# Kernel tuning notes

Measured on AMD Instinct MI355X. Metric: run time of the kernel, lower is better.

The kernel has to match this reference:

```python
import jax, jax.numpy as jnp
import numpy as np

GAMMA = 1.0

def setup_inputs() -> dict:
    key = jax.random.key(0)
    kq, kk, kv = jax.random.split(key, 3)
    B, N, M, D = 4, 2048, 2048, 128
    q = jax.random.normal(kq, (B, N, D), dtype=jnp.float32)
    k = jax.random.normal(kk, (B, M, D), dtype=jnp.float32)
    v = jax.random.normal(kv, (B, M, D), dtype=jnp.float32)
    return {"q": q, "k": k, "v": v}

def reference(q, k, v):
    # RBF attention: weights = softmax(-gamma * ||q_i - k_j||^2, axis=-1)
    # dist2 via expansion ||q||^2 + ||k||^2 - 2 q.k (same math as broadcast-subtract,
    # avoids materializing the [B,N,M,D] tensor the torch code builds).
    q2 = jnp.sum(q * q, axis=-1)                    # [B,N]
    k2 = jnp.sum(k * k, axis=-1)                    # [B,M]
    qk = jnp.einsum('bnd,bmd->bnm', q, k)           # [B,N,M]
    dist2 = q2[:, :, None] + k2[:, None, :] - 2.0 * qk
    weights = jax.nn.softmax(-GAMMA * dist2, axis=-1)  # [B,N,M]
    return jnp.einsum('bnm,bmd->bnd', weights, v)      # [B,N,D]
```

## Files before the change

kernel.cpp:

```cpp
#include <hip/hip_runtime.h>
#include <hip/hip_bf16.h>

#define B_ 4
#define N_ 2048
#define M_ 2048
#define D_ 128
#define QBLK 128
#define NTHREADS 256
#define KVBLK 64
#define NTILES 32
#define TILE_BYTES 16384
#define SPLIT_MAX 8

typedef __attribute__((ext_vector_type(8))) short short8;
typedef __attribute__((ext_vector_type(16))) float floatx16;
typedef __attribute__((ext_vector_type(4))) unsigned int u32x4;
typedef unsigned short u16;
typedef unsigned int u32;

__device__ __forceinline__ u16 f2bf(float x) {
  u32 u = __builtin_bit_cast(u32, x);
  u32 r = (u + 0x7FFFu + ((u >> 16) & 1u)) >> 16;
  return (u16)r;
}
__device__ __forceinline__ float bf2f(u16 h) {
  u32 u = ((u32)h) << 16;
  return __builtin_bit_cast(float, u);
}
__device__ __forceinline__ u32 cvtpk(float a, float b) {
  u32 r;
  asm("v_cvt_pk_bf16_f32 %0, %1, %2" : "=v"(r) : "v"(a), "v"(b));
  return r;
}

#define GLOAD16(src, dst)                                                     \
  __builtin_amdgcn_global_load_lds(                                           \
      (const __attribute__((address_space(1))) void*)(src),                   \
      (__attribute__((address_space(3))) void*)(dst), 16, 0, 0)

__global__ __launch_bounds__(256) void prep_kernel(
    const float* __restrict__ k, const float* __restrict__ v,
    u16* __restrict__ khi_g, u16* __restrict__ klo_g,
    u16* __restrict__ vt_g, float* __restrict__ k2_g)
{
  __shared__ u16 T[64][136];
  int tid = threadIdx.x;
  if (blockIdx.x < 512) {
    int gid = blockIdx.x * 256 + tid;
    int row_g = gid >> 4;
    int j = gid & 15;
    const float* kp = k + (size_t)row_g * D_ + j * 8;
    float4 a = *(const float4*)kp;
    float4 c = *(const float4*)(kp + 4);
    float xs[8] = {a.x, a.y, a.z, a.w, c.x, c.y, c.z, c.w};
    short8 hi, lo;
    float ss = 0.f;
    #pragma unroll
    for (int e = 0; e < 8; ++e) {
      ss += xs[e] * xs[e];
      float x2 = 2.f * xs[e];
      u16 h = f2bf(x2);
      hi[e] = (short)h;
      lo[e] = (short)f2bf(x2 - bf2f(h));
    }
    ss += __shfl_xor(ss, 1);
    ss += __shfl_xor(ss, 2);
    ss += __shfl_xor(ss, 4);
    ss += __shfl_xor(ss, 8);
    if (j == 0) k2_g[row_g] = ss;
    int m = row_g & (M_ - 1);
    int b = row_g >> 11;
    int tile = m >> 6, r = m & 63;
    size_t base = ((size_t)b * NTILES + tile) * TILE_BYTES;
    u32 off = (u32)(r * 256 + j * 16) ^ ((u32)(r & 7) << 4);
    *(short8*)((char*)khi_g + base + off) = hi;
    *(short8*)((char*)klo_g + base + off) = lo;
  } else {
    int blk = blockIdx.x - 512;
    int b = blk >> 5, tile = blk & 31;
    const float* vp = v + ((size_t)b * M_ + tile * 64) * D_;
    #pragma unroll
    for (int p = 0; p < 8; ++p) {
      int idx = p * 256 + tid;
      int r = idx >> 5, c4 = idx & 31;
      float4 vv = *(const float4*)(vp + (size_t)r * D_ + c4 * 4);
      T[r][c4 * 4 + 0] = f2bf(vv.x);
      T[r][c4 * 4 + 1] = f2bf(vv.y);
      T[r][c4 * 4 + 2] = f2bf(vv.z);
      T[r][c4 * 4 + 3] = f2bf(vv.w);
    }
    __syncthreads();
    size_t base = ((size_t)b * NTILES + tile) * TILE_BYTES;
    #pragma unroll
    for (int p = 0; p < 4; ++p) {
      int idx = p * 256 + tid;
      int d = idx >> 3, rb = idx & 7;
      short8 s;
      #pragma unroll
      for (int i = 0; i < 8; ++i) s[i] = (short)T[rb * 8 + i][d];
      u32 off = (u32)(d * 128 + rb * 16) ^ ((u32)(d & 7) << 4);
      *(short8*)((char*)vt_g + base + off) = s;
    }
  }
}

__global__ __launch_bounds__(NTHREADS, 2) void rbf_attn_kernel(
    const float* __restrict__ q, const u16* __restrict__ khi_g,
    const u16* __restrict__ klo_g, const u16* __restrict__ vt_g,
    const float* __restrict__ k2_g, float* __restrict__ out,
    float* __restrict__ Opart, float* __restrict__ mpart,
    float* __restrict__ lpart, int nsplit, int tiles_per_split)
{
  __shared__ __align__(16) u16 KhiL[64 * 128];
  __shared__ __align__(16) u16 KloL[64 * 128];
  __shared__ __align__(16) u16 VtL[128 * 64];
  __shared__ __align__(16) float k2L[64];

  const int tid = threadIdx.x;
  const int w = tid >> 6;
  const int lane = tid & 63;
  const int qlc = lane & 31;
  const int h = lane >> 5;
  const int b = blockIdx.y;
  const int qt = blockIdx.x;
  const int sp = blockIdx.z;
  const int q0 = qt * QBLK;
  const int kt0 = sp * tiles_per_split, kt1 = kt0 + tiles_per_split;

  short8 Qh[8], Ql[8];
  {
    const float* qp = q + ((size_t)b * N_ + q0 + w * 32 + qlc) * D_ + h * 8;
    #pragma unroll
    for (int s = 0; s < 8; ++s) {
      float4 a = *(const float4*)(qp + s * 16);
      float4 c = *(const float4*)(qp + s * 16 + 4);
      float xs[8] = {a.x, a.y, a.z, a.w, c.x, c.y, c.z, c.w};
      #pragma unroll
      for (int j = 0; j < 8; ++j) {
        u16 hi = f2bf(xs[j]);
        Qh[s][j] = (short)hi;
        Ql[s][j] = (short)f2bf(xs[j] - bf2f(hi));
      }
    }
  }

  const char* khi_b = (const char*)khi_g + (size_t)b * NTILES * TILE_BYTES;
  const char* klo_b = (const char*)klo_g + (size_t)b * NTILES * TILE_BYTES;
  const char* vt_b = (const char*)vt_g + (size_t)b * NTILES * TILE_BYTES;
  const float* k2_b = k2_g + (size_t)b * M_;

  floatx16 o[4];
  #pragma unroll
  for (int dt = 0; dt < 4; ++dt) o[dt] = (floatx16)0.0f;
  float mrun = -1e30f, lrun = 0.f;

  for (int kt = kt0; kt < kt1; ++kt) {
    __syncthreads();
    {
      const char* kh = khi_b + (size_t)kt * TILE_BYTES;
      const char* kl = klo_b + (size_t)kt * TILE_BYTES;
      const char* vt = vt_b + (size_t)kt * TILE_BYTES;
      const int so = tid * 16;
      #pragma unroll
      for (int c = 0; c < 4; ++c) {
        GLOAD16(kh + c * 4096 + so, (char*)KhiL + c * 4096 + w * 1024);
        GLOAD16(kl + c * 4096 + so, (char*)KloL + c * 4096 + w * 1024);
        GLOAD16(vt + c * 4096 + so, (char*)VtL + c * 4096 + w * 1024);
      }
      if (tid < 16)
        GLOAD16((const char*)(k2_b + kt * KVBLK) + tid * 16, (char*)k2L);
    }
    asm volatile("s_waitcnt vmcnt(0)" ::: "memory");
    __syncthreads();

    floatx16 accS0 = (floatx16)0.0f, accS1 = (floatx16)0.0f;
    __builtin_amdgcn_s_setprio(1);
    #pragma unroll
    for (int s = 0; s < 8; ++s) {
      {
        int row = qlc;
        u32 off = ((u32)(row * 256 + s * 32 + h * 16)) ^ ((u32)(row & 7) << 4);
        short8 ah = *(const short8*)((const char*)KhiL + off);
        short8 al = *(const short8*)((const char*)KloL + off);
        accS0 = __builtin_amdgcn_mfma_f32_32x32x16_bf16(ah, Qh[s], accS0, 0, 0, 0);
        accS0 = __builtin_amdgcn_mfma_f32_32x32x16_bf16(al, Qh[s], accS0, 0, 0, 0);
        accS0 = __builtin_amdgcn_mfma_f32_32x32x16_bf16(ah, Ql[s], accS0, 0, 0, 0);
      }
      {
        int row = 32 + qlc;
        u32 off = ((u32)(row * 256 + s * 32 + h * 16)) ^ ((u32)(row & 7) << 4);
        short8 ah = *(const short8*)((const char*)KhiL + off);
        short8 al = *(const short8*)((const char*)KloL + off);
        accS1 = __builtin_amdgcn_mfma_f32_32x32x16_bf16(ah, Qh[s], accS1, 0, 0, 0);
        accS1 = __builtin_amdgcn_mfma_f32_32x32x16_bf16(al, Qh[s], accS1, 0, 0, 0);
        accS1 = __builtin_amdgcn_mfma_f32_32x32x16_bf16(ah, Ql[s], accS1, 0, 0, 0);
      }
    }
    __builtin_amdgcn_s_setprio(0);

    float mx = -3e38f;
    #pragma unroll
    for (int ct = 0; ct < 2; ++ct) {
      #pragma unroll
      for (int g = 0; g < 4; ++g) {
        float4 kq = *(const float4*)&k2L[32 * ct + 8 * g + 4 * h];
        if (ct == 0) {
          accS0[4 * g + 0] -= kq.x; accS0[4 * g + 1] -= kq.y;
          accS0[4 * g + 2] -= kq.z; accS0[4 * g + 3] -= kq.w;
          mx = fmaxf(mx, fmaxf(fmaxf(accS0[4 * g], accS0[4 * g + 1]),
                               fmaxf(accS0[4 * g + 2], accS0[4 * g + 3])));
        } else {
          accS1[4 * g + 0] -= kq.x; accS1[4 * g + 1] -= kq.y;
          accS1[4 * g + 2] -= kq.z; accS1[4 * g + 3] -= kq.w;
          mx = fmaxf(mx, fmaxf(fmaxf(accS1[4 * g], accS1[4 * g + 1]),
                               fmaxf(accS1[4 * g + 2], accS1[4 * g + 3])));
        }
      }
    }
    mx = fmaxf(mx, __shfl_xor(mx, 32));
    if (!__all(mx - mrun <= 8.f)) {
      float mnew = fmaxf(mrun, mx);
      float scl = __expf(mrun - mnew);
      mrun = mnew;
      lrun *= scl;
      #pragma unroll
      for (int i = 0; i < 16; ++i) {
        o[0][i] *= scl; o[1][i] *= scl; o[2][i] *= scl; o[3][i] *= scl;
      }
    }
    float ls = 0.f;
    u32 W[2][4][2];
    #pragma unroll
    for (int ct = 0; ct < 2; ++ct) {
      #pragma unroll
      for (int g = 0; g < 4; ++g) {
        float p0, p1, p2, p3;
        if (ct == 0) {
          p0 = __expf(accS0[4 * g + 0] - mrun); p1 = __expf(accS0[4 * g + 1] - mrun);
          p2 = __expf(accS0[4 * g + 2] - mrun); p3 = __expf(accS0[4 * g + 3] - mrun);
        } else {
          p0 = __expf(accS1[4 * g + 0] - mrun); p1 = __expf(accS1[4 * g + 1] - mrun);
          p2 = __expf(accS1[4 * g + 2] - mrun); p3 = __expf(accS1[4 * g + 3] - mrun);
        }
        ls += (p0 + p1) + (p2 + p3);
        W[ct][g][0] = cvtpk(p0, p1);
        W[ct][g][1] = cvtpk(p2, p3);
      }
    }
    ls += __shfl_xor(ls, 32);
    lrun += ls;

    u32 X[2][4][2];
    #pragma unroll
    for (int ct = 0; ct < 2; ++ct)
      #pragma unroll
      for (int g = 0; g < 4; ++g) {
        X[ct][g][0] = __shfl_xor(W[ct][g][0], 32);
        X[ct][g][1] = __shfl_xor(W[ct][g][1], 32);
      }

    const bool h0 = (h == 0);
    __builtin_amdgcn_s_setprio(1);
    #pragma unroll
    for (int s2 = 0; s2 < 4; ++s2) {
      const int ct = s2 >> 1, e = s2 & 1;
      u32 w0 = h0 ? W[ct][2 * e][0] : X[ct][2 * e + 1][0];
      u32 w1 = h0 ? W[ct][2 * e][1] : X[ct][2 * e + 1][1];
      u32 w2 = h0 ? X[ct][2 * e][0] : W[ct][2 * e + 1][0];
      u32 w3 = h0 ? X[ct][2 * e][1] : W[ct][2 * e + 1][1];
      short8 pf = __builtin_bit_cast(short8, (u32x4){w0, w1, w2, w3});
      #pragma unroll
      for (int dt = 0; dt < 4; ++dt) {
        int row = dt * 32 + qlc;
        u32 off = ((u32)(row * 128 + s2 * 32 + h * 16)) ^ ((u32)(row & 7) << 4);
        short8 af = *(const short8*)((const char*)VtL + off);
        o[dt] = __builtin_amdgcn_mfma_f32_32x32x16_bf16(af, pf, o[dt], 0, 0, 0);
      }
    }
    __builtin_amdgcn_s_setprio(0);
  }

  const int qt32 = qt * 4 + w;
  if (nsplit == 1) {
    float inv = 1.0f / lrun;
    float* ob = out + ((size_t)b * N_ + q0 + w * 32 + qlc) * D_;
    #pragma unroll
    for (int dt = 0; dt < 4; ++dt)
      #pragma unroll
      for (int r = 0; r < 16; ++r) {
        int d = dt * 32 + (r & 3) + 8 * (r >> 2) + 4 * h;
        ob[d] = o[dt][r] * inv;
      }
  } else {
    float* ob = Opart + ((((size_t)sp * B_ + b) * (N_ / 32) + qt32) * D_) * 32;
    #pragma unroll
    for (int dt = 0; dt < 4; ++dt)
      #pragma unroll
      for (int r = 0; r < 16; ++r) {
        int d = dt * 32 + (r & 3) + 8 * (r >> 2) + 4 * h;
        ob[(size_t)d * 32 + qlc] = o[dt][r];
      }
    if (h == 0) {
      size_t mrow = ((size_t)sp * B_ + b) * N_ + qt32 * 32 + qlc;
      mpart[mrow] = mrun;
      lpart[mrow] = lrun;
    }
  }
}

__global__ __launch_bounds__(256) void rbf_reduce_kernel(
    const float* __restrict__ Opart, const float* __restrict__ mpart,
    const float* __restrict__ lpart, float* __restrict__ out, int nsplit)
{
  __shared__ float T[32][136];
  const int t = threadIdx.x;
  const int qln = t & 31, dg = t >> 5;
  const int b = blockIdx.x >> 6, qt32 = blockIdx.x & 63;
  const size_t stride = (size_t)B_ * N_;
  const size_t mbase = (size_t)b * N_ + qt32 * 32 + qln;
  float mmax = -3e38f;
  for (int s = 0; s < nsplit; ++s)
    mmax = fmaxf(mmax, mpart[s * stride + mbase]);
  float acc[16];
  #pragma unroll
  for (int i = 0; i < 16; ++i) acc[i] = 0.f;
  float lsum = 0.f;
  for (int s = 0; s < nsplit; ++s) {
    float wv = __expf(mpart[s * stride + mbase] - mmax);
    lsum += wv * lpart[s * stride + mbase];
    const float* ob = Opart +
        ((((size_t)s * B_ + b) * (N_ / 32) + qt32) * D_ + dg * 16) * 32 + qln;
    #pragma unroll
    for (int dd = 0; dd < 16; ++dd) acc[dd] += wv * ob[(size_t)dd * 32];
  }
  float inv = 1.0f / lsum;
  #pragma unroll
  for (int dd = 0; dd < 16; ++dd) T[qln][dg * 16 + dd] = acc[dd] * inv;
  __syncthreads();
  const int r = t >> 3, seg = t & 7;
  float* op = out + ((size_t)b * N_ + qt32 * 32 + r) * D_ + seg * 16;
  #pragma unroll
  for (int i = 0; i < 4; ++i) {
    float4 v4 = {T[r][seg * 16 + 4 * i], T[r][seg * 16 + 4 * i + 1],
                 T[r][seg * 16 + 4 * i + 2], T[r][seg * 16 + 4 * i + 3]};
    *(float4*)(op + 4 * i) = v4;
  }
}

extern "C" void kernel_launch(void* const* d_in, const int* in_sizes, int n_in,
                              void* d_out, int out_size, void* d_ws, size_t ws_size,
                              hipStream_t stream) {
  const float* q = (const float*)d_in[0];
  const float* k = (const float*)d_in[1];
  const float* v = (const float*)d_in[2];
  float* out = (float*)d_out;

  const size_t tileBytesAll = (size_t)B_ * NTILES * TILE_BYTES;
  u16* khi_g = (u16*)d_ws;
  u16* klo_g = (u16*)((char*)d_ws + tileBytesAll);
  u16* vt_g  = (u16*)((char*)d_ws + 2 * tileBytesAll);
  float* k2_g = (float*)((char*)d_ws + 3 * tileBytesAll);
  const size_t prepBytes = 3 * tileBytesAll + (size_t)B_ * M_ * sizeof(float);

  const size_t perO = (size_t)B_ * N_ * D_ * sizeof(float);
  const size_t perML = 2 * (size_t)B_ * N_ * sizeof(float);
  int nsplit = SPLIT_MAX;
  while (nsplit > 1 && prepBytes + (size_t)nsplit * (perO + perML) > ws_size)
    nsplit >>= 1;

  float* Opart = (float*)((char*)d_ws + prepBytes);
  float* mpart = Opart + (size_t)nsplit * B_ * N_ * D_;
  float* lpart = mpart + (size_t)nsplit * B_ * N_;
  int tiles_per_split = NTILES / nsplit;

  prep_kernel<<<512 + B_ * NTILES, 256, 0, stream>>>(k, v, khi_g, klo_g, vt_g,
                                                     k2_g);

  dim3 grid(N_ / QBLK, B_, nsplit);
  rbf_attn_kernel<<<grid, NTHREADS, 0, stream>>>(
      q, khi_g, klo_g, vt_g, k2_g, out, Opart, mpart, lpart, nsplit,
      tiles_per_split);
  if (nsplit > 1) {
    rbf_reduce_kernel<<<B_ * (N_ / 32), 256, 0, stream>>>(
        Opart, mpart, lpart, out, nsplit);
  }
}
```

Before: 44.43 us.

## Use exp2 softmax, bf16 split partials, and XCD-aware block mapping

Folds log2(e) into the prepared K and k2 values so the softmax uses exp2 directly, with the rescale-defer threshold adjusted to match. Split-K partial outputs are stored as bf16 instead of fp32, halving the partial-output write and read traffic in the reduce step. The attention grid is flattened and remapped so that blocks sharing a batch and split land on the same XCD, improving L2 reuse of K/V tiles. The bf16 partials add rounding error to the combined output.

```diff
diff --git a/kernel.cpp b/kernel.cpp
--- a/kernel.cpp
+++ b/kernel.cpp
@@ -11,6 +11,9 @@
 #define NTILES 32
 #define TILE_BYTES 16384
 #define SPLIT_MAX 8
+#define SCALE2LOG 2.885390081777927f
+#define LOG2E 1.4426950408889634f
+#define DEFER_THR 11.5424f
 
 typedef __attribute__((ext_vector_type(8))) short short8;
 typedef __attribute__((ext_vector_type(16))) float floatx16;
@@ -58,7 +61,7 @@
     #pragma unroll
     for (int e = 0; e < 8; ++e) {
       ss += xs[e] * xs[e];
-      float x2 = 2.f * xs[e];
+      float x2 = SCALE2LOG * xs[e];
       u16 h = f2bf(x2);
       hi[e] = (short)h;
       lo[e] = (short)f2bf(x2 - bf2f(h));
@@ -67,7 +70,7 @@
     ss += __shfl_xor(ss, 2);
     ss += __shfl_xor(ss, 4);
     ss += __shfl_xor(ss, 8);
-    if (j == 0) k2_g[row_g] = ss;
+    if (j == 0) k2_g[row_g] = ss * LOG2E;
     int m = row_g & (M_ - 1);
     int b = row_g >> 11;
     int tile = m >> 6, r = m & 63;
@@ -108,7 +111,7 @@
     const float* __restrict__ q, const u16* __restrict__ khi_g,
     const u16* __restrict__ klo_g, const u16* __restrict__ vt_g,
     const float* __restrict__ k2_g, float* __restrict__ out,
-    float* __restrict__ Opart, float* __restrict__ mpart,
+    u16* __restrict__ Opart, float* __restrict__ mpart,
     float* __restrict__ lpart, int nsplit, int tiles_per_split)
 {
   __shared__ __align__(16) u16 KhiL[64 * 128];
@@ -121,9 +124,24 @@
   const int lane = tid & 63;
   const int qlc = lane & 31;
   const int h = lane >> 5;
-  const int b = blockIdx.y;
-  const int qt = blockIdx.x;
-  const int sp = blockIdx.z;
+
+  int b, qi, sp;
+  {
+    int gid = blockIdx.x;
+    if (nsplit >= 2) {
+      int xcd = gid & 7, slot = gid >> 3;
+      int gpx = nsplit >> 1;
+      int group = xcd * gpx + (slot >> 4);
+      qi = slot & 15;
+      b = group & 3;
+      sp = group >> 2;
+    } else {
+      qi = gid & 15;
+      b = gid >> 4;
+      sp = 0;
+    }
+  }
+  const int qt = qi;
   const int q0 = qt * QBLK;
   const int kt0 = sp * tiles_per_split, kt1 = kt0 + tiles_per_split;
 
@@ -218,9 +236,9 @@
       }
     }
     mx = fmaxf(mx, __shfl_xor(mx, 32));
-    if (!__all(mx - mrun <= 8.f)) {
+    if (!__all(mx - mrun <= DEFER_THR)) {
       float mnew = fmaxf(mrun, mx);
-      float scl = __expf(mrun - mnew);
+      float scl = exp2f(mrun - mnew);
       mrun = mnew;
       lrun *= scl;
       #pragma unroll
@@ -236,11 +254,11 @@
       for (int g = 0; g < 4; ++g) {
         float p0, p1, p2, p3;
         if (ct == 0) {
-          p0 = __expf(accS0[4 * g + 0] - mrun); p1 = __expf(accS0[4 * g + 1] - mrun);
-          p2 = __expf(accS0[4 * g + 2] - mrun); p3 = __expf(accS0[4 * g + 3] - mrun);
+          p0 = exp2f(accS0[4 * g + 0] - mrun); p1 = exp2f(accS0[4 * g + 1] - mrun);
+          p2 = exp2f(accS0[4 * g + 2] - mrun); p3 = exp2f(accS0[4 * g + 3] - mrun);
         } else {
-          p0 = __expf(accS1[4 * g + 0] - mrun); p1 = __expf(accS1[4 * g + 1] - mrun);
-          p2 = __expf(accS1[4 * g + 2] - mrun); p3 = __expf(accS1[4 * g + 3] - mrun);
+          p0 = exp2f(accS1[4 * g + 0] - mrun); p1 = exp2f(accS1[4 * g + 1] - mrun);
+          p2 = exp2f(accS1[4 * g + 2] - mrun); p3 = exp2f(accS1[4 * g + 3] - mrun);
         }
         ls += (p0 + p1) + (p2 + p3);
         W[ct][g][0] = cvtpk(p0, p1);
@@ -292,13 +310,13 @@
         ob[d] = o[dt][r] * inv;
       }
   } else {
-    float* ob = Opart + ((((size_t)sp * B_ + b) * (N_ / 32) + qt32) * D_) * 32;
+    u16* ob = Opart + ((((size_t)sp * B_ + b) * (N_ / 32) + qt32) * D_) * 32;
     #pragma unroll
     for (int dt = 0; dt < 4; ++dt)
       #pragma unroll
       for (int r = 0; r < 16; ++r) {
         int d = dt * 32 + (r & 3) + 8 * (r >> 2) + 4 * h;
-        ob[(size_t)d * 32 + qlc] = o[dt][r];
+        ob[(size_t)d * 32 + qlc] = f2bf(o[dt][r]);
       }
     if (h == 0) {
       size_t mrow = ((size_t)sp * B_ + b) * N_ + qt32 * 32 + qlc;
@@ -309,7 +327,7 @@
 }
 
 __global__ __launch_bounds__(256) void rbf_reduce_kernel(
-    const float* __restrict__ Opart, const float* __restrict__ mpart,
+    const u16* __restrict__ Opart, const float* __restrict__ mpart,
     const float* __restrict__ lpart, float* __restrict__ out, int nsplit)
 {
   __shared__ float T[32][136];
@@ -326,12 +344,12 @@
   for (int i = 0; i < 16; ++i) acc[i] = 0.f;
   float lsum = 0.f;
   for (int s = 0; s < nsplit; ++s) {
-    float wv = __expf(mpart[s * stride + mbase] - mmax);
+    float wv = exp2f(mpart[s * stride + mbase] - mmax);
     lsum += wv * lpart[s * stride + mbase];
-    const float* ob = Opart +
+    const u16* ob = Opart +
         ((((size_t)s * B_ + b) * (N_ / 32) + qt32) * D_ + dg * 16) * 32 + qln;
     #pragma unroll
-    for (int dd = 0; dd < 16; ++dd) acc[dd] += wv * ob[(size_t)dd * 32];
+    for (int dd = 0; dd < 16; ++dd) acc[dd] += wv * bf2f(ob[(size_t)dd * 32]);
   }
   float inv = 1.0f / lsum;
   #pragma unroll
@@ -362,22 +380,21 @@
   float* k2_g = (float*)((char*)d_ws + 3 * tileBytesAll);
   const size_t prepBytes = 3 * tileBytesAll + (size_t)B_ * M_ * sizeof(float);
 
-  const size_t perO = (size_t)B_ * N_ * D_ * sizeof(float);
+  const size_t perO = (size_t)B_ * N_ * D_ * sizeof(u16);
   const size_t perML = 2 * (size_t)B_ * N_ * sizeof(float);
   int nsplit = SPLIT_MAX;
   while (nsplit > 1 && prepBytes + (size_t)nsplit * (perO + perML) > ws_size)
     nsplit >>= 1;
 
-  float* Opart = (float*)((char*)d_ws + prepBytes);
-  float* mpart = Opart + (size_t)nsplit * B_ * N_ * D_;
+  u16* Opart = (u16*)((char*)d_ws + prepBytes);
+  float* mpart = (float*)((char*)d_ws + prepBytes + (size_t)nsplit * perO);
   float* lpart = mpart + (size_t)nsplit * B_ * N_;
   int tiles_per_split = NTILES / nsplit;
 
   prep_kernel<<<512 + B_ * NTILES, 256, 0, stream>>>(k, v, khi_g, klo_g, vt_g,
                                                      k2_g);
 
-  dim3 grid(N_ / QBLK, B_, nsplit);
-  rbf_attn_kernel<<<grid, NTHREADS, 0, stream>>>(
+  rbf_attn_kernel<<<dim3(16 * B_ * nsplit), NTHREADS, 0, stream>>>(
       q, khi_g, klo_g, vt_g, k2_g, out, Opart, mpart, lpart, nsplit,
       tiles_per_split);
   if (nsplit > 1) {
```

Result: no change. 44.94 us (+1.1%).
